# Optimization experiments

Measured on AMD Instinct MI355X. Metric: run time of the kernel, lower is better.

## Reference

```python
import jax, jax.numpy as jnp
import numpy as np

B, L_IN, D_MODEL, CONV_D, KSIZE = 16, 512, 384, 1536, 3
MEL_MAX = 4096
LN_EPS = 1e-5


def _conv1d_same(h, w, b):
    # h: [B, C_in, L], w: [C_out, C_in, K] -> [B, C_out, L]
    y = jax.lax.conv_general_dilated(h, w, window_strides=(1,), padding='SAME',
                                     dimension_numbers=('NCH', 'OIH', 'NCH'))
    return y + b[None, :, None]


def _layernorm(x, g, b):
    m = jnp.mean(x, -1, keepdims=True)
    v = jnp.mean((x - m) ** 2, -1, keepdims=True)
    return (x - m) * jax.lax.rsqrt(v + LN_EPS) * g + b


def _ffn(x, wa, ba, wb, bb):
    # Conv1D_FFT: conv(d_model->conv_d) ReLU conv(conv_d->d_model) ReLU
    h = jnp.transpose(x, (0, 2, 1))
    h = jax.nn.relu(_conv1d_same(h, wa, ba))
    h = jax.nn.relu(_conv1d_same(h, wb, bb))
    return jnp.transpose(h, (0, 2, 1))


def _dur_pred(x, w1, b1, w2, b2, g1, be1, w3, b3, w4, b4, g2, be2, wl, bl):
    h = _ffn(x, w1, b1, w2, b2)
    h = _layernorm(h, g1, be1)  # dropout is identity at eval
    h = _ffn(h, w3, b3, w4, b4)
    h = _layernorm(h, g2, be2)
    return (h @ wl + bl)[..., 0]  # [B, L_in], squeeze(-1)


def _length_regulate(x, dur, mel_max_len):
    # Equivalent to alignment @ x where alignment[b,t,j]=1 iff cum[b,j-1] <= t < cum[b,j],
    # padded with zeros out to mel_max_len (original pads output to mel_max_len).
    cum = jnp.cumsum(dur, axis=-1)                        # [B, L_in]
    total = cum[:, -1]                                    # [B]
    t = jnp.arange(mel_max_len, dtype=cum.dtype)          # [T]
    idx = jax.vmap(lambda c: jnp.searchsorted(c, t, side='right'))(cum)  # [B, T]
    idx = jnp.minimum(idx, x.shape[1] - 1)
    out = jnp.take_along_axis(x, idx[:, :, None], axis=1)  # [B, T, D]
    mask = (t[None, :] < total[:, None])[..., None]
    return out * mask


def setup_inputs() -> dict:
    key = jax.random.key(0)
    ks = jax.random.split(key, 8)
    def nrm(k, shape):
        return jax.random.normal(k, shape, jnp.float32) * 0.02
    return {
        'x': jax.random.normal(ks[0], (B, L_IN, D_MODEL), jnp.float32),
        'target': jax.random.randint(ks[1], (B, L_IN), 0, 8, jnp.int32),
        'mel_max_len': MEL_MAX,
        'w1': nrm(ks[2], (CONV_D, D_MODEL, KSIZE)), 'b1': jnp.zeros((CONV_D,), jnp.float32),
        'w2': nrm(ks[3], (D_MODEL, CONV_D, KSIZE)), 'b2': jnp.zeros((D_MODEL,), jnp.float32),
        'g1': jnp.ones((D_MODEL,), jnp.float32), 'be1': jnp.zeros((D_MODEL,), jnp.float32),
        'w3': nrm(ks[4], (CONV_D, D_MODEL, KSIZE)), 'b3': jnp.zeros((CONV_D,), jnp.float32),
        'w4': nrm(ks[5], (D_MODEL, CONV_D, KSIZE)), 'b4': jnp.zeros((D_MODEL,), jnp.float32),
        'g2': jnp.ones((D_MODEL,), jnp.float32), 'be2': jnp.zeros((D_MODEL,), jnp.float32),
        'wl': nrm(ks[6], (D_MODEL, 1)), 'bl': jnp.zeros((1,), jnp.float32),
    }


def reference(x, target, mel_max_len, w1, b1, w2, b2, g1, be1, w3, b3, w4, b4, g2, be2, wl, bl):
    dur_preds = _dur_pred(x, w1, b1, w2, b2, g1, be1, w3, b3, w4, b4, g2, be2, wl, bl)
    output = _length_regulate(x, target, mel_max_len)
    return (output, dur_preds)
```

## Files before the change

kernel.cpp:

```cpp
#include <hip/hip_runtime.h>
#include <hip/hip_bf16.h>
#include <cstddef>
#include <cstdint>

#define NB 16
#define LIN 512
#define DM 384
#define DC 1536
#define MELMAX 4096
#define LN_EPS 1e-5f

typedef __bf16 bf16x8 __attribute__((ext_vector_type(8)));
typedef float f32x4 __attribute__((ext_vector_type(4)));

#define GL2LDS(gp, lp)                                                                \
    __builtin_amdgcn_global_load_lds((const __attribute__((address_space(1))) void*)(gp), \
                                     (__attribute__((address_space(3))) void*)(lp), 16, 0, 0)

__device__ __forceinline__ float wred(float v) {
#pragma unroll
    for (int m = 32; m >= 1; m >>= 1) v += __shfl_xor(v, m, 64);
    return v;
}

__device__ __forceinline__ unsigned short f2bf(float f) {
    __hip_bfloat16 h = __float2bfloat16(f);
    return *reinterpret_cast<unsigned short*>(&h);
}

__device__ __forceinline__ float bf2f(unsigned short u) {
    return __uint_as_float(((unsigned)u) << 16);
}


__global__ __launch_bounds__(256) void gather_kernel(const float* __restrict__ x,
                                                     const int* __restrict__ cum,
                                                     float* __restrict__ out) {
    const int wid = (blockIdx.x * 256 + threadIdx.x) >> 6;
    const int lane = threadIdx.x & 63;
    const int b = wid >> 12;
    const int t = wid & (MELMAX - 1);
    const int* c = cum + b * LIN;
    const int total = c[LIN - 1];
    float4* orow = reinterpret_cast<float4*>(out + ((size_t)b * MELMAX + t) * DM);
    if (t < total) {
        int lo = 0, hi = LIN;
        while (lo < hi) { int mid = (lo + hi) >> 1; if (c[mid] > t) hi = mid; else lo = mid + 1; }
        const int idx = lo < (LIN - 1) ? lo : (LIN - 1);
        const float4* xrow = reinterpret_cast<const float4*>(x + ((size_t)b * LIN + idx) * DM);
#pragma unroll
        for (int j = 0; j < 2; ++j) {
            const int p = lane + 64 * j;
            if (p < DM / 4) orow[p] = xrow[p];
        }
    } else {
        const float4 z = make_float4(0.f, 0.f, 0.f, 0.f);
#pragma unroll
        for (int j = 0; j < 2; ++j) {
            const int p = lane + 64 * j;
            if (p < DM / 4) orow[p] = z;
        }
    }
}


#define ZPAD_BLKS 96
#define CASTX_BLKS 3072
#define WCAST_BLKS 288
#define PREP_TOTAL (ZPAD_BLKS + CASTX_BLKS + 4 * WCAST_BLKS + NB)

__global__ void prep_kernel(const float* __restrict__ x, unsigned short* __restrict__ xb,
                            unsigned short* __restrict__ hbig, unsigned short* __restrict__ h2b,
                            const float* __restrict__ w1, const float* __restrict__ w2,
                            const float* __restrict__ w3, const float* __restrict__ w4,
                            unsigned short* __restrict__ o1, unsigned short* __restrict__ o2,
                            unsigned short* __restrict__ o3, unsigned short* __restrict__ o4,
                            const int* __restrict__ tgt, int* __restrict__ cum) {
    const int bid = blockIdx.x, tid = threadIdx.x;
    if (bid < ZPAD_BLKS) {
        const int buf = bid >> 5, rem = bid & 31;
        const int b = rem >> 1, row = (rem & 1) ? (LIN + 1) : 0;
        unsigned short* p = buf == 0 ? xb : (buf == 1 ? hbig : h2b);
        const int rl = buf == 1 ? DC : DM;
        unsigned short* base = p + ((size_t)b * (LIN + 2) + row) * rl;
        for (int c = tid; c < rl; c += 256) base[c] = 0;
        return;
    }
    if (bid < ZPAD_BLKS + CASTX_BLKS) {
        const int idx = (bid - ZPAD_BLKS) * 256 + tid;
        const float4 v = reinterpret_cast<const float4*>(x)[idx];
        const int e = idx * 4;
        const int b = e / (LIN * DM);
        const int rem = e - b * (LIN * DM);
        const int l = rem / DM;
        const int c = rem - l * DM;
        ushort4 o;
        o.x = f2bf(v.x); o.y = f2bf(v.y); o.z = f2bf(v.z); o.w = f2bf(v.w);
        *reinterpret_cast<ushort4*>(xb + ((size_t)b * (LIN + 2) + l + 1) * DM + c) = o;
        return;
    }
    if (bid < ZPAD_BLKS + CASTX_BLKS + 4 * WCAST_BLKS) {
        const int j = bid - ZPAD_BLKS - CASTX_BLKS;
        const int which = j / WCAST_BLKS;
        const int idx = (j - which * WCAST_BLKS) * 256 + tid;
        const float* w = which == 0 ? w1 : which == 1 ? w2 : which == 2 ? w3 : w4;
        unsigned short* gg = which == 0 ? o1 : which == 1 ? o2 : which == 2 ? o3 : o4;
        const int CI = (which == 0 || which == 2) ? DM : DC;
        const int OCT = CI / 8;
        const int co = idx / OCT, ci0 = (idx - co * OCT) * 8;
        const float4* p4 = reinterpret_cast<const float4*>(w + (size_t)(co * CI + ci0) * 3);
        float v[24];
#pragma unroll
        for (int q = 0; q < 6; ++q) *reinterpret_cast<float4*>(&v[q * 4]) = p4[q];
        unsigned short tmp[3][8];
#pragma unroll
        for (int e = 0; e < 24; ++e) tmp[e % 3][e / 3] = f2bf(v[e]);
        unsigned short* ob = gg + (size_t)co * (3 * CI) + ci0;
#pragma unroll
        for (int t = 0; t < 3; ++t)
            *reinterpret_cast<uint4*>(ob + (size_t)t * CI) = *reinterpret_cast<const uint4*>(tmp[t]);
        return;
    }
    {
        const int b = bid - (ZPAD_BLKS + CASTX_BLKS + 4 * WCAST_BLKS);
        __shared__ int s[LIN];
        s[tid] = tgt[b * LIN + tid];
        s[tid + 256] = tgt[b * LIN + tid + 256];
        __syncthreads();
        for (int off = 1; off < LIN; off <<= 1) {
            int v0 = (tid >= off) ? s[tid - off] : 0;
            int v1 = (tid + 256 >= off) ? s[tid + 256 - off] : 0;
            __syncthreads();
            s[tid] += v0;
            s[tid + 256] += v1;
            __syncthreads();
        }
        cum[b * LIN + tid] = s[tid];
        cum[b * LIN + tid + 256] = s[tid + 256];
    }
}


template <int CI, int CO, int BN>
__global__ __launch_bounds__(256, 2) void conv_mfma_kernel(const unsigned short* __restrict__ in,
                                                           const unsigned short* __restrict__ wg,
                                                           const float* __restrict__ bias,
                                                           unsigned short* __restrict__ out) {
    constexpr int BM = 128, BK = 32;
    constexpr int KC = CI / BK;
    constexpr int AGRP = 12;
    constexpr int GPT = BN / 16;
    constexpr int BGRP = 3 * GPT;
    constexpr int NW_N = BN / 32;
    constexpr int NT = CO / BN;
    constexpr int NCONV = NB * (LIN / BM) * NT;

    __shared__ __align__(16) unsigned short As[2][AGRP * 512];
    __shared__ __align__(16) unsigned short Bs[2][BGRP * 512];

    const int tid = threadIdx.x;
    const int lane = tid & 63;
    const int wv = tid >> 6;

    const int orig = blockIdx.x;
    const int q = NCONV >> 3, xcd = orig & 7, o = orig >> 3;
    const int wgid = xcd * q + o;

    const int mg = wgid / NT;
    const int nt = wgid - mg * NT;
    const int b = mg >> 2;
    const int l0 = (mg & 3) * BM;
    const int n0 = nt * BN;

    const int wr = wv >> 1, wc = wv & 1;

    const unsigned short* inb = in + (size_t)b * (LIN + 2) * CI;

    f32x4 acc[4][NW_N];
#pragma unroll
    for (int m = 0; m < 4; ++m)
#pragma unroll
        for (int n = 0; n < NW_N; ++n) acc[m][n] = (f32x4){0.f, 0.f, 0.f, 0.f};

    const int lrow = lane >> 2;
    const int lch = lane & 3;
    const int fr = lane & 15, kg = lane >> 4;

    const unsigned short* aroot = inb + (size_t)l0 * CI + lch * 8;
    const unsigned short* broot = wg + (size_t)n0 * (3 * CI) + lch * 8;

#define STAGE(c, kb)                                                                      \
    do {                                                                                  \
        const unsigned short* abase = aroot + (kb) * BK;                                  \
        _Pragma("unroll")                                                                 \
        for (int g = wv; g < AGRP; g += 4) {                                              \
            const int sg = g < 9 ? g : 0;    \
            GL2LDS(abase + (size_t)(sg * 16 + lrow) * CI, &As[c][g * 512]);               \
        }                                                                                 \
        const unsigned short* bbase = broot + (kb) * BK;                                  \
        _Pragma("unroll")                                                                 \
        for (int g2 = wv; g2 < BGRP; g2 += 4) {                                           \
            const int t = g2 / GPT, gr = g2 - t * GPT;                                    \
            GL2LDS(bbase + (size_t)(gr * 16 + lrow) * (3 * CI) + (size_t)t * CI,          \
                   &Bs[c][g2 * 512]);                                                     \
        }                                                                                 \
    } while (0)

#define COMPUTE(c)                                                                        \
    do {                                                                                  \
        _Pragma("unroll")                                                                 \
        for (int t = 0; t < 3; ++t) {                                                     \
            bf16x8 aF[4], bF[NW_N];                                                       \
            _Pragma("unroll")                                                             \
            for (int m = 0; m < 4; ++m)                                                   \
                aF[m] = *reinterpret_cast<const bf16x8*>(                                 \
                    &As[c][(t + wr * 64 + m * 16 + fr) * BK + kg * 8]);                   \
            _Pragma("unroll")                                                             \
            for (int n = 0; n < NW_N; ++n)                                                \
                bF[n] = *reinterpret_cast<const bf16x8*>(                                 \
                    &Bs[c][(t * BN + wc * (BN / 2) + n * 16 + fr) * BK + kg * 8]);        \
            _Pragma("unroll")                                                             \
            for (int m = 0; m < 4; ++m)                                                   \
                _Pragma("unroll")                                                         \
                for (int n = 0; n < NW_N; ++n)                                            \
                    acc[m][n] =                                                           \
                        __builtin_amdgcn_mfma_f32_16x16x32_bf16(aF[m], bF[n], acc[m][n],  \
                                                                0, 0, 0);                 \
        }                                                                                 \
    } while (0)

    STAGE(0, 0);
    STAGE(1, 1);
#pragma unroll 1
    for (int kb = 0; kb < KC; ++kb) {
        const int cur = kb & 1;
        if constexpr (BN == 128)
            asm volatile("s_waitcnt vmcnt(9)" ::: "memory");
        else
            asm volatile("s_waitcnt vmcnt(6)" ::: "memory");
        __builtin_amdgcn_sched_barrier(0);
        __builtin_amdgcn_s_barrier();
        __builtin_amdgcn_sched_barrier(0);
        COMPUTE(cur);
        asm volatile("s_waitcnt lgkmcnt(0)" ::: "memory");
        __builtin_amdgcn_sched_barrier(0);
        __builtin_amdgcn_s_barrier();
        __builtin_amdgcn_sched_barrier(0);
        int nk = kb + 2;
        if (nk >= KC) nk -= KC;
        STAGE(cur, nk);
    }
#undef STAGE
#undef COMPUTE
    asm volatile("s_waitcnt vmcnt(0)" ::: "memory");

    const int fq = lane >> 4;
    float bv[NW_N];
#pragma unroll
    for (int n = 0; n < NW_N; ++n) bv[n] = bias[n0 + wc * (BN / 2) + n * 16 + fr];
    unsigned short* outb = out + (size_t)b * (LIN + 2) * CO;
#pragma unroll
    for (int m = 0; m < 4; ++m)
#pragma unroll
        for (int qy = 0; qy < 4; ++qy) {
            const int grow = l0 + wr * 64 + m * 16 + fq * 4 + qy + 1;
            unsigned short* orow = outb + (size_t)grow * CO + n0 + wc * (BN / 2) + fr;
#pragma unroll
            for (int n = 0; n < NW_N; ++n) {
                const float v = fmaxf(acc[m][n][qy] + bv[n], 0.f);
                orow[n * 16] = f2bf(v);
            }
        }
}


__global__ __launch_bounds__(256) void ln_kernel(unsigned short* __restrict__ h,
                                                 const float* __restrict__ g,
                                                 const float* __restrict__ be) {
    const int row = blockIdx.x * 4 + (threadIdx.x >> 6);
    const int lane = threadIdx.x & 63;
    const int b = row >> 9, l = row & (LIN - 1);
    unsigned short* hr = h + ((size_t)b * (LIN + 2) + l + 1) * DM;
    float v[6];
    float s = 0.f;
#pragma unroll
    for (int j = 0; j < 6; ++j) { v[j] = bf2f(hr[lane + 64 * j]); s += v[j]; }
    s = wred(s);
    const float mean = s * (1.f / DM);
    float vs = 0.f;
#pragma unroll
    for (int j = 0; j < 6; ++j) { const float d = v[j] - mean; vs += d * d; }
    vs = wred(vs);
    const float rstd = rsqrtf(vs * (1.f / DM) + LN_EPS);
#pragma unroll
    for (int j = 0; j < 6; ++j) {
        const int c = lane + 64 * j;
        hr[c] = f2bf((v[j] - mean) * rstd * g[c] + be[c]);
    }
}


__global__ __launch_bounds__(256) void ln_linear_kernel(const unsigned short* __restrict__ h,
                                                        const float* __restrict__ g,
                                                        const float* __restrict__ be,
                                                        const float* __restrict__ wl,
                                                        const float* __restrict__ bl,
                                                        float* __restrict__ dur) {
    const int row = blockIdx.x * 4 + (threadIdx.x >> 6);
    const int lane = threadIdx.x & 63;
    const int b = row >> 9, l = row & (LIN - 1);
    const unsigned short* hr = h + ((size_t)b * (LIN + 2) + l + 1) * DM;
    float v[6];
    float s = 0.f;
#pragma unroll
    for (int j = 0; j < 6; ++j) { v[j] = bf2f(hr[lane + 64 * j]); s += v[j]; }
    s = wred(s);
    const float mean = s * (1.f / DM);
    float vs = 0.f;
#pragma unroll
    for (int j = 0; j < 6; ++j) { const float d = v[j] - mean; vs += d * d; }
    vs = wred(vs);
    const float rstd = rsqrtf(vs * (1.f / DM) + LN_EPS);
    float dot = 0.f;
#pragma unroll
    for (int j = 0; j < 6; ++j) {
        const int c = lane + 64 * j;
        dot += ((v[j] - mean) * rstd * g[c] + be[c]) * wl[c];
    }
    dot = wred(dot);
    if (lane == 0) dur[row] = dot + bl[0];
}


extern "C" void kernel_launch(void* const* d_in, const int* in_sizes, int n_in,
                              void* d_out, int out_size, void* d_ws, size_t ws_size,
                              hipStream_t stream) {
    const float* x   = (const float*)d_in[0];
    const int*   tgt = (const int*)d_in[1];
    const float* w1  = (const float*)d_in[3];
    const float* b1  = (const float*)d_in[4];
    const float* w2  = (const float*)d_in[5];
    const float* b2  = (const float*)d_in[6];
    const float* g1  = (const float*)d_in[7];
    const float* be1 = (const float*)d_in[8];
    const float* w3  = (const float*)d_in[9];
    const float* b3  = (const float*)d_in[10];
    const float* w4  = (const float*)d_in[11];
    const float* b4  = (const float*)d_in[12];
    const float* g2  = (const float*)d_in[13];
    const float* be2 = (const float*)d_in[14];
    const float* wl  = (const float*)d_in[15];
    const float* bl  = (const float*)d_in[16];

    float* out = (float*)d_out;
    float* dur = out + (size_t)NB * MELMAX * DM;

    unsigned short* ws = (unsigned short*)d_ws;
    unsigned short* xb   = ws;
    unsigned short* hbig = xb + (size_t)NB * (LIN + 2) * DM;
    unsigned short* h2b  = hbig + (size_t)NB * (LIN + 2) * DC;
    unsigned short* wg1  = h2b + (size_t)NB * (LIN + 2) * DM;
    unsigned short* wg2  = wg1 + (size_t)DC * 3 * DM;
    unsigned short* wg3  = wg2 + (size_t)DM * 3 * DC;
    unsigned short* wg4  = wg3 + (size_t)DC * 3 * DM;
    int* cum = (int*)(wg4 + (size_t)DM * 3 * DC);

    prep_kernel<<<PREP_TOTAL, 256, 0, stream>>>(x, xb, hbig, h2b, w1, w2, w3, w4,
                                                wg1, wg2, wg3, wg4, tgt, cum);

    gather_kernel<<<(NB * MELMAX) / 4, 256, 0, stream>>>(x, cum, out);

    conv_mfma_kernel<DM, DC, 128><<<NB * (LIN / 128) * (DC / 128), 256, 0, stream>>>(xb, wg1, b1, hbig);
    conv_mfma_kernel<DC, DM, 64><<<NB * (LIN / 128) * (DM / 64), 256, 0, stream>>>(hbig, wg2, b2, h2b);
    ln_kernel<<<NB * LIN / 4, 256, 0, stream>>>(h2b, g1, be1);
    conv_mfma_kernel<DM, DC, 128><<<NB * (LIN / 128) * (DC / 128), 256, 0, stream>>>(h2b, wg3, b3, hbig);
    conv_mfma_kernel<DC, DM, 64><<<NB * (LIN / 128) * (DM / 64), 256, 0, stream>>>(hbig, wg4, b4, xb);
    ln_linear_kernel<<<NB * LIN / 4, 256, 0, stream>>>(xb, g2, be2, wl, bl, dur);
}
```

Before: 220.8 us.

## Add 256x256-tile 8-wave conv kernel for the d_model-to-conv_d convolutions

Adds a new conv kernel for the two DM->DC convolutions. It uses 512 threads, a 256x256 output tile, 64-wide K chunks with XOR-swizzled LDS staging and a ping-pong schedule. Barriers and setprio are interleaved between quarter-tile MFMA groups so that loads overlap compute, and block indices are remapped to group blocks in the grid. The larger tile is meant to raise reuse per LDS load and MFMA utilisation compared with the 128x128 tiles. In exchange it uses 128KB of LDS and many accumulator registers, which may limit occupancy, and the grid has only 192 blocks.

```diff
diff --git a/kernel.cpp b/kernel.cpp
--- a/kernel.cpp
+++ b/kernel.cpp
@@ -141,6 +141,165 @@
 }
 
 
+__global__ __launch_bounds__(512, 2) void conv8_kernel(const unsigned short* __restrict__ in,
+                                                       const unsigned short* __restrict__ wg,
+                                                       const float* __restrict__ bias,
+                                                       unsigned short* __restrict__ out) {
+    constexpr int NKT = 18;
+    __shared__ __align__(16) unsigned short smem[65536];
+
+    const int tid = threadIdx.x, lane = tid & 63, wv = tid >> 6;
+    const int wrM = wv >> 2, wcN = wv & 3;
+
+    const int orig = blockIdx.x;
+    const int wgid = (orig & 7) * 24 + (orig >> 3);
+    const int mt = wgid / 6, ng = wgid - mt * 6;
+    const int b = mt >> 1, tm = mt & 1;
+    const int n0 = ng * 256;
+
+    const unsigned short* inb = in + ((size_t)b * (LIN + 2) + (size_t)tm * 256) * DM;
+
+    const int fr = lane & 15, kg = lane >> 4;
+
+    f32x4 acc[8][4];
+#pragma unroll
+    for (int i = 0; i < 8; ++i)
+#pragma unroll
+        for (int j = 0; j < 4; ++j) acc[i][j] = (f32x4){0.f, 0.f, 0.f, 0.f};
+
+#define STG_A(s, H, kt)                                                                   \
+    do {                                                                                  \
+        const int t_ = (kt) / 6, kc_ = (kt) - t_ * 6;                                     \
+        _Pragma("unroll")                                                                 \
+        for (int j = 0; j < 2; ++j) {                                                     \
+            const int rr = (tid >> 3) + j * 64;                                           \
+            const int e = ((tid & 7) * 8) ^ ((rr & 4) << 2);                              \
+            GL2LDS(inb + (size_t)(t_ + (H)*128 + rr) * DM + kc_ * 64 + e,                 \
+                   smem + (s)*32768 + (H)*8192 + tid * 8 + j * 4096);                     \
+        }                                                                                 \
+    } while (0)
+
+#define STG_B(s, H, kt)                                                                   \
+    do {                                                                                  \
+        const int t_ = (kt) / 6, kc_ = (kt) - t_ * 6;                                     \
+        _Pragma("unroll")                                                                 \
+        for (int j = 0; j < 2; ++j) {                                                     \
+            const int rr = (tid >> 3) + j * 64;                                           \
+            const int e = ((tid & 7) * 8) ^ ((rr & 4) << 2);                              \
+            GL2LDS(wg + (size_t)(n0 + (H)*128 + rr) * 1152 + t_ * 384 + kc_ * 64 + e,     \
+                   smem + (s)*32768 + 16384 + (H)*8192 + tid * 8 + j * 4096);             \
+        }                                                                                 \
+    } while (0)
+
+#define LDA(mh, s)                                                                        \
+    do {                                                                                  \
+        _Pragma("unroll")                                                                 \
+        for (int mf = 0; mf < 4; ++mf)                                                    \
+            _Pragma("unroll")                                                             \
+            for (int kh = 0; kh < 2; ++kh) {                                              \
+                const int rr = (mh)*64 + mf * 16 + fr;                                    \
+                const int ke = (kh * 32 + kg * 8) ^ ((rr & 4) << 2);                      \
+                aF[mf][kh] = *reinterpret_cast<const bf16x8*>(                            \
+                    smem + (s)*32768 + wrM * 8192 + rr * 64 + ke);                        \
+            }                                                                             \
+    } while (0)
+
+#define LDB(nh, s)                                                                        \
+    do {                                                                                  \
+        _Pragma("unroll")                                                                 \
+        for (int nf = 0; nf < 2; ++nf)                                                    \
+            _Pragma("unroll")                                                             \
+            for (int kh = 0; kh < 2; ++kh) {                                              \
+                const int rr = wcN * 32 + nf * 16 + fr;                                   \
+                const int ke = (kh * 32 + kg * 8) ^ ((rr & 4) << 2);                      \
+                bF[nf][kh] = *reinterpret_cast<const bf16x8*>(                            \
+                    smem + (s)*32768 + 16384 + (nh)*8192 + rr * 64 + ke);                 \
+            }                                                                             \
+    } while (0)
+
+#define MMA(mh, nh)                                                                       \
+    do {                                                                                  \
+        _Pragma("unroll")                                                                 \
+        for (int mf = 0; mf < 4; ++mf)                                                    \
+            _Pragma("unroll")                                                             \
+            for (int nf = 0; nf < 2; ++nf)                                                \
+                _Pragma("unroll")                                                         \
+                for (int kh = 0; kh < 2; ++kh)                                            \
+                    acc[(mh)*4 + mf][(nh)*2 + nf] = __builtin_amdgcn_mfma_f32_16x16x32_bf16( \
+                        aF[mf][kh], bF[nf][kh], acc[(mh)*4 + mf][(nh)*2 + nf], 0, 0, 0);  \
+    } while (0)
+
+    STG_A(0, 0, 0); STG_A(0, 1, 0); STG_B(0, 0, 0); STG_B(0, 1, 0);
+    STG_B(1, 0, 1); STG_B(1, 1, 1);
+    asm volatile("s_waitcnt vmcnt(4)" ::: "memory");
+    asm volatile("s_barrier" ::: "memory");
+
+#pragma unroll 1
+    for (int m = 0; m < NKT; ++m) {
+        const int s = m & 1, s1 = s ^ 1;
+        int k1 = m + 1; if (k1 >= NKT) k1 -= NKT;
+        int k2 = m + 2; if (k2 >= NKT) k2 -= NKT;
+        bf16x8 aF[4][2], bF[2][2];
+        LDA(0, s); LDB(0, s);
+        STG_A(s1, 0, k1);
+        asm volatile("s_barrier" ::: "memory");
+        asm volatile("s_waitcnt lgkmcnt(0)" ::: "memory");
+        __builtin_amdgcn_s_setprio(1); MMA(0, 0); __builtin_amdgcn_s_setprio(0);
+        asm volatile("s_barrier" ::: "memory");
+        LDA(1, s);
+        STG_B(s, 0, k2);
+        asm volatile("s_barrier" ::: "memory");
+        asm volatile("s_waitcnt lgkmcnt(0)" ::: "memory");
+        __builtin_amdgcn_s_setprio(1); MMA(1, 0); __builtin_amdgcn_s_setprio(0);
+        asm volatile("s_barrier" ::: "memory");
+        LDB(1, s);
+        STG_A(s1, 1, k1);
+        asm volatile("s_barrier" ::: "memory");
+        asm volatile("s_waitcnt lgkmcnt(0)" ::: "memory");
+        __builtin_amdgcn_s_setprio(1); MMA(1, 1); __builtin_amdgcn_s_setprio(0);
+        asm volatile("s_barrier" ::: "memory");
+        LDA(0, s);
+        STG_B(s, 1, k2);
+        asm volatile("s_barrier" ::: "memory");
+        asm volatile("s_waitcnt lgkmcnt(0)" ::: "memory");
+        __builtin_amdgcn_s_setprio(1); MMA(0, 1); __builtin_amdgcn_s_setprio(0);
+        asm volatile("s_waitcnt vmcnt(2)" ::: "memory");
+        asm volatile("s_barrier" ::: "memory");
+    }
+#undef STG_A
+#undef STG_B
+#undef LDA
+#undef LDB
+#undef MMA
+    asm volatile("s_waitcnt vmcnt(0)" ::: "memory");
+
+    const int fq = lane >> 4;
+    float bv[4];
+#pragma unroll
+    for (int nh = 0; nh < 2; ++nh)
+#pragma unroll
+        for (int nf = 0; nf < 2; ++nf)
+            bv[nh * 2 + nf] = bias[n0 + nh * 128 + wcN * 32 + nf * 16 + fr];
+    unsigned short* outb = out + ((size_t)b * (LIN + 2) + (size_t)tm * 256 + 1) * DC;
+#pragma unroll
+    for (int mh = 0; mh < 2; ++mh)
+#pragma unroll
+        for (int mf = 0; mf < 4; ++mf)
+#pragma unroll
+            for (int qy = 0; qy < 4; ++qy) {
+                const int r = wrM * 128 + mh * 64 + mf * 16 + fq * 4 + qy;
+                unsigned short* orow = outb + (size_t)r * DC + n0;
+#pragma unroll
+                for (int nh = 0; nh < 2; ++nh)
+#pragma unroll
+                    for (int nf = 0; nf < 2; ++nf) {
+                        const float v = fmaxf(acc[mh * 4 + mf][nh * 2 + nf][qy] + bv[nh * 2 + nf], 0.f);
+                        orow[nh * 128 + wcN * 32 + nf * 16 + fr] = f2bf(v);
+                    }
+            }
+}
+
+
 template <int CI, int CO, int BN>
 __global__ __launch_bounds__(256, 2) void conv_mfma_kernel(const unsigned short* __restrict__ in,
                                                            const unsigned short* __restrict__ wg,
@@ -194,7 +353,7 @@
         const unsigned short* abase = aroot + (kb) * BK;                                  \
         _Pragma("unroll")                                                                 \
         for (int g = wv; g < AGRP; g += 4) {                                              \
-            const int sg = g < 9 ? g : 0;    \
+            const int sg = g < 9 ? g : 0;                                                 \
             GL2LDS(abase + (size_t)(sg * 16 + lrow) * CI, &As[c][g * 512]);               \
         }                                                                                 \
         const unsigned short* bbase = broot + (kb) * BK;                                  \
@@ -370,10 +529,10 @@
 
     gather_kernel<<<(NB * MELMAX) / 4, 256, 0, stream>>>(x, cum, out);
 
-    conv_mfma_kernel<DM, DC, 128><<<NB * (LIN / 128) * (DC / 128), 256, 0, stream>>>(xb, wg1, b1, hbig);
+    conv8_kernel<<<NB * 2 * (DC / 256), 512, 0, stream>>>(xb, wg1, b1, hbig);
     conv_mfma_kernel<DC, DM, 64><<<NB * (LIN / 128) * (DM / 64), 256, 0, stream>>>(hbig, wg2, b2, h2b);
     ln_kernel<<<NB * LIN / 4, 256, 0, stream>>>(h2b, g1, be1);
-    conv_mfma_kernel<DM, DC, 128><<<NB * (LIN / 128) * (DC / 128), 256, 0, stream>>>(h2b, wg3, b3, hbig);
+    conv8_kernel<<<NB * 2 * (DC / 256), 512, 0, stream>>>(h2b, wg3, b3, hbig);
     conv_mfma_kernel<DC, DM, 64><<<NB * (LIN / 128) * (DM / 64), 256, 0, stream>>>(hbig, wg4, b4, xb);
     ln_linear_kernel<<<NB * LIN / 4, 256, 0, stream>>>(xb, g2, be2, wl, bl, dur);
 }
```

After: 216.8 us. About the same (-1.8%).
